# Kernel tuning notes

Measured on AMD Instinct MI355X. Metric: run time of the kernel, lower is better.

## Reference

```python
import jax, jax.numpy as jnp
import numpy as np

B, T, E, H, V = 64, 21, 512, 512, 10000


def _lstm_step(x, h, c, W_ih, W_hh, b):
    # PyTorch LSTMCell gate order: i, f, g, o
    gates = x @ W_ih.T + h @ W_hh.T + b  # [B, 4H]
    i, f, g, o = jnp.split(gates, 4, axis=-1)
    i, f, o = jax.nn.sigmoid(i), jax.nn.sigmoid(f), jax.nn.sigmoid(o)
    g = jnp.tanh(g)
    c_new = f * c + i * g
    h_new = o * jnp.tanh(c_new)
    return h_new, c_new


def setup_inputs() -> dict:
    key = jax.random.key(0)
    ks = jax.random.split(key, 8)
    s_ih = 1.0 / np.sqrt(H)
    return {
        "features": jax.random.normal(ks[0], (B, E), jnp.float32),
        "caption_embedding": jax.random.normal(ks[1], (B, T, E), jnp.float32),
        "W_ih": jax.random.uniform(ks[2], (4 * H, E), jnp.float32, -s_ih, s_ih),
        "W_hh": jax.random.uniform(ks[3], (4 * H, H), jnp.float32, -s_ih, s_ih),
        "b_ih": jax.random.uniform(ks[4], (4 * H,), jnp.float32, -s_ih, s_ih),
        "b_hh": jax.random.uniform(ks[5], (4 * H,), jnp.float32, -s_ih, s_ih),
        "W_lin": jax.random.uniform(ks[6], (V, H), jnp.float32, -s_ih, s_ih),
        "b_lin": jax.random.uniform(ks[7], (V,), jnp.float32, -s_ih, s_ih),
    }


def reference(features, caption_embedding, W_ih, W_hh, b_ih, b_hh, W_lin, b_lin):
    b = b_ih + b_hh
    batch = features.shape[0]
    hidden = W_hh.shape[1]
    h0 = jnp.zeros((batch, hidden), features.dtype)
    c0 = jnp.zeros((batch, hidden), features.dtype)
    # t = 0: consume image features, no output emitted
    h, c = _lstm_step(features, h0, c0, W_ih, W_hh, b)
    # t = 1..T-1: consume caption_embedding[:, t-1], emit linear(h)
    emb_seq = jnp.swapaxes(caption_embedding[:, :-1, :], 0, 1)  # [T-1, B, E]

    def body(carry, x_t):
        h, c = carry
        h, c = _lstm_step(x_t, h, c, W_ih, W_hh, b)
        out = h @ W_lin.T + b_lin  # [B, V]
        return (h, c), out

    _, outs = jax.lax.scan(body, (h, c), emb_seq)  # [T-1, B, V]
    return jnp.swapaxes(outs, 0, 1)  # [B, T-1, V]
```

## Files before the change

kernel.cpp:

```cpp
#include <hip/hip_runtime.h>
#include <hip/hip_bf16.h>


#define NB 64
#define NT 21
#define NE 512
#define NH 512
#define NV 10000
#define G4 2048
#define FLGD 16

typedef __attribute__((ext_vector_type(8))) short bf16x8;
typedef __attribute__((ext_vector_type(4))) float f32x4;
typedef __attribute__((ext_vector_type(4))) unsigned short u16x4;

#define OFF_WIH_HI   0UL
#define OFF_WIH_LO   2097152UL
#define OFF_WHH_HI   4194304UL
#define OFF_WHH_LO   6291456UL
#define OFF_WLIN_HI  8388608UL
#define OFF_XSEQ_HI  18743296UL
#define OFF_XSEQ_LO  20185088UL
#define OFF_BIAS     21626880UL
#define OFF_XIH      21635072UL
#define OFF_GHH      32645120UL
#define OFF_GHL      32776192UL
#define OFF_C        32907264UL
#define OFF_HBUF     33038336UL
#define OFF_FLG      34349056UL

__device__ inline unsigned short f2bf(float f) {
    unsigned int u = __float_as_uint(f);
    unsigned int r = u + 0x7FFFu + ((u >> 16) & 1u);
    return (unsigned short)(r >> 16);
}
__device__ inline float bf2f(unsigned short s) {
    return __uint_as_float(((unsigned int)s) << 16);
}

__device__ __forceinline__ void gl_lds16(const unsigned short* g, unsigned short* l) {
    auto gp = (const __attribute__((address_space(1))) unsigned int*)(unsigned long long)(const void*)g;
    auto lp = (__attribute__((address_space(3))) unsigned int*)(unsigned int)(unsigned long long)(void*)l;
    __builtin_amdgcn_global_load_lds(gp, lp, 16, 0, 0);
}

__device__ __forceinline__ void gl_lds16_sc(const unsigned short* g, unsigned short* l) {
    auto gp = (const __attribute__((address_space(1))) unsigned int*)(unsigned long long)(const void*)g;
    auto lp = (__attribute__((address_space(3))) unsigned int*)(unsigned int)(unsigned long long)(void*)l;
    __builtin_amdgcn_global_load_lds(gp, lp, 16, 0, 17);
}

__device__ __forceinline__ void st4_sc(unsigned int* p, unsigned int v) {
    asm volatile("global_store_dword %0, %1, off sc0 sc1" :: "v"(p), "v"(v) : "memory");
}

__global__ __launch_bounds__(256) void prep_kernel(
    const float* __restrict__ features, const float* __restrict__ cap,
    const float* __restrict__ W_ih, const float* __restrict__ W_hh,
    const float* __restrict__ b_ih, const float* __restrict__ b_hh,
    const float* __restrict__ W_lin, unsigned char* __restrict__ ws)
{
    const int idx = blockIdx.x * 256 + threadIdx.x;
    unsigned short* wih_hi = (unsigned short*)(ws + OFF_WIH_HI);
    unsigned short* wih_lo = (unsigned short*)(ws + OFF_WIH_LO);
    unsigned short* whh_hi = (unsigned short*)(ws + OFF_WHH_HI);
    unsigned short* whh_lo = (unsigned short*)(ws + OFF_WHH_LO);
    unsigned short* wlin_hi = (unsigned short*)(ws + OFF_WLIN_HI);
    unsigned short* xs_hi = (unsigned short*)(ws + OFF_XSEQ_HI);
    unsigned short* xs_lo = (unsigned short*)(ws + OFF_XSEQ_LO);
    float* bias = (float*)(ws + OFF_BIAS);

    if (idx < 262144) {
        const int i4 = idx * 4;
        float4 w = *(const float4*)(W_ih + i4);
        u16x4 hi, lo;
        hi.x = f2bf(w.x); lo.x = f2bf(w.x - bf2f(hi.x));
        hi.y = f2bf(w.y); lo.y = f2bf(w.y - bf2f(hi.y));
        hi.z = f2bf(w.z); lo.z = f2bf(w.z - bf2f(hi.z));
        hi.w = f2bf(w.w); lo.w = f2bf(w.w - bf2f(hi.w));
        *(u16x4*)(wih_hi + i4) = hi;
        *(u16x4*)(wih_lo + i4) = lo;
    } else if (idx < 524288) {
        const int i4 = (idx - 262144) * 4;
        float4 w = *(const float4*)(W_hh + i4);
        u16x4 hi, lo;
        hi.x = f2bf(w.x); lo.x = f2bf(w.x - bf2f(hi.x));
        hi.y = f2bf(w.y); lo.y = f2bf(w.y - bf2f(hi.y));
        hi.z = f2bf(w.z); lo.z = f2bf(w.z - bf2f(hi.z));
        hi.w = f2bf(w.w); lo.w = f2bf(w.w - bf2f(hi.w));
        *(u16x4*)(whh_hi + i4) = hi;
        *(u16x4*)(whh_lo + i4) = lo;
    } else if (idx < 1804288) {
        const int i4 = (idx - 524288) * 4;
        float4 w = *(const float4*)(W_lin + i4);
        u16x4 hi;
        hi.x = f2bf(w.x); hi.y = f2bf(w.y); hi.z = f2bf(w.z); hi.w = f2bf(w.w);
        *(u16x4*)(wlin_hi + i4) = hi;
    } else if (idx < 1976320) {
        const int i4 = (idx - 1804288) * 4;
        const int e = i4 & 511;
        const int b = (i4 >> 9) & 63;
        const int t = i4 >> 15;
        float4 x = (t == 0) ? *(const float4*)(features + b * NE + e)
                            : *(const float4*)(cap + b * (NT * NE) + (t - 1) * NE + e);
        u16x4 hi, lo;
        hi.x = f2bf(x.x); lo.x = f2bf(x.x - bf2f(hi.x));
        hi.y = f2bf(x.y); lo.y = f2bf(x.y - bf2f(hi.y));
        hi.z = f2bf(x.z); lo.z = f2bf(x.z - bf2f(hi.z));
        hi.w = f2bf(x.w); lo.w = f2bf(x.w - bf2f(hi.w));
        *(u16x4*)(xs_hi + i4) = hi;
        *(u16x4*)(xs_lo + i4) = lo;
    } else if (idx < 1976832) {
        const int j = (idx - 1976320) * 4;
        float4 a = *(const float4*)(b_ih + j);
        float4 b = *(const float4*)(b_hh + j);
        *(float4*)(bias + j) = make_float4(a.x + b.x, a.y + b.y, a.z + b.z, a.w + b.w);
    }
}

__global__ __launch_bounds__(256) void gemm_a_kernel(unsigned char* __restrict__ ws)
{
    __shared__ unsigned short Ah[2][4096], Al[2][4096], Bh[2][4096], Bl[2][4096];
    const int tid = threadIdx.x;
    const int lane = tid & 63, wv = tid >> 6;
    const int mf = lane & 15, kg = lane >> 4;
    const int mw = (wv >> 1) * 64, nw = (wv & 1) * 64;
    const int m0 = blockIdx.y * 128, n0 = blockIdx.x * 128;

    const unsigned short* __restrict__ xh = (const unsigned short*)(ws + OFF_XSEQ_HI);
    const unsigned short* __restrict__ xl = (const unsigned short*)(ws + OFF_XSEQ_LO);
    const unsigned short* __restrict__ wh = (const unsigned short*)(ws + OFF_WIH_HI);
    const unsigned short* __restrict__ wl = (const unsigned short*)(ws + OFF_WIH_LO);
    const float* __restrict__ bias = (const float*)(ws + OFF_BIAS);
    float* __restrict__ xih = (float*)(ws + OFF_XIH);

    f32x4 acc[4][4];
#pragma unroll
    for (int i = 0; i < 4; i++)
#pragma unroll
        for (int j = 0; j < 4; j++) acc[i][j] = (f32x4){0.f, 0.f, 0.f, 0.f};

    auto stage = [&](int buf, int k0) {
#pragma unroll
        for (int h = 0; h < 2; ++h) {
            int s = h * 256 + tid;
            int r = s >> 2, ks = (s & 3) * 8;
            gl_lds16(xh + (size_t)(m0 + r) * 512 + k0 + ks, &Ah[buf][s * 8]);
            gl_lds16(xl + (size_t)(m0 + r) * 512 + k0 + ks, &Al[buf][s * 8]);
            gl_lds16(wh + (size_t)(n0 + r) * 512 + k0 + ks, &Bh[buf][s * 8]);
            gl_lds16(wl + (size_t)(n0 + r) * 512 + k0 + ks, &Bl[buf][s * 8]);
        }
    };

    stage(0, 0);
    for (int kt = 0; kt < 16; ++kt) {
        __syncthreads();
        const int cur = kt & 1;
        if (kt < 15) stage(cur ^ 1, (kt + 1) * 32);
        bf16x8 ah[4], al[4], bh[4], bl[4];
#pragma unroll
        for (int i = 0; i < 4; i++) {
            ah[i] = *(const bf16x8*)&Ah[cur][(mw + i * 16 + mf) * 32 + kg * 8];
            al[i] = *(const bf16x8*)&Al[cur][(mw + i * 16 + mf) * 32 + kg * 8];
            bh[i] = *(const bf16x8*)&Bh[cur][(nw + i * 16 + mf) * 32 + kg * 8];
            bl[i] = *(const bf16x8*)&Bl[cur][(nw + i * 16 + mf) * 32 + kg * 8];
        }
#pragma unroll
        for (int i = 0; i < 4; i++)
#pragma unroll
            for (int j = 0; j < 4; j++) {
                acc[i][j] = __builtin_amdgcn_mfma_f32_16x16x32_bf16(ah[i], bh[j], acc[i][j], 0, 0, 0);
                acc[i][j] = __builtin_amdgcn_mfma_f32_16x16x32_bf16(ah[i], bl[j], acc[i][j], 0, 0, 0);
                acc[i][j] = __builtin_amdgcn_mfma_f32_16x16x32_bf16(al[i], bh[j], acc[i][j], 0, 0, 0);
            }
    }
#pragma unroll
    for (int i = 0; i < 4; i++)
#pragma unroll
        for (int j = 0; j < 4; j++) {
            const int col = n0 + nw + j * 16 + mf;
            const float bb = bias[col];
#pragma unroll
            for (int r = 0; r < 4; r++) {
                const int R = m0 + mw + i * 16 + kg * 4 + r;
                if (R < NT * NB) xih[(size_t)R * G4 + col] = acc[i][j][r] + bb;
            }
        }
}

__global__ __launch_bounds__(512, 2) void fused_persistent(
    unsigned char* __restrict__ ws, const float* __restrict__ b_lin, float* __restrict__ out)
{
    __shared__ unsigned short Hhi[64 * 512];
    __shared__ unsigned short Hlo[64 * 512];
    __shared__ float glf[4096];
    const int tid = threadIdx.x;
    const int lane = tid & 63, wv = tid >> 6;
    const int mf = lane & 15, kg = lane >> 4;

    unsigned int* __restrict__ flg = (unsigned int*)(ws + OFF_C);
    unsigned short* __restrict__ hbuf = (unsigned short*)(ws + OFF_HBUF);
    const unsigned short* __restrict__ wlin = (const unsigned short*)(ws + OFF_WLIN_HI);

    if (blockIdx.x < 32) {
        const int bc = blockIdx.x;
        const int q = wv & 3;
        const int mh = wv >> 2;

        unsigned short* __restrict__ ghh = (unsigned short*)(ws + OFF_GHH);
        unsigned short* __restrict__ ghl = (unsigned short*)(ws + OFF_GHL);
        const unsigned short* __restrict__ whh_hi = (const unsigned short*)(ws + OFF_WHH_HI);
        const unsigned short* __restrict__ whh_lo = (const unsigned short*)(ws + OFF_WHH_LO);
        const float* __restrict__ xih_base = (const float*)(ws + OFF_XIH);

        bf16x8 bh[16], blo[16];
#pragma unroll
        for (int j = 0; j < 16; ++j) {
            const size_t off = (size_t)(q * 512 + bc * 16 + mf) * 512 + j * 32 + kg * 8;
            bh[j] = *(const bf16x8*)(whh_hi + off);
            blo[j] = *(const bf16x8*)(whh_lo + off);
        }

        const int crow = tid >> 3;
        const int cp = tid & 7;
        const int c0 = bc * 16 + cp * 2;
        const int jc0 = c0 >> 3;
        float creg0 = 0.f, creg1 = 0.f;

        float2 xp[4];
        auto load_xp = [&](int tt) {
            const float* __restrict__ xq = xih_base + (size_t)tt * NB * G4;
#pragma unroll
            for (int g2 = 0; g2 < 4; ++g2)
                xp[g2] = *(const float2*)&xq[crow * G4 + g2 * 512 + c0];
        };
        load_xp(0);

        for (int t = 0; t < NT; ++t) {
            f32x4 acc[2];
            acc[0] = (f32x4){0.f, 0.f, 0.f, 0.f};
            acc[1] = (f32x4){0.f, 0.f, 0.f, 0.f};

            if (t > 0) {
                const int rd = (t + 1) & 1;
                const unsigned short* __restrict__ ghh_r = ghh + rd * (NB * NH);
                const unsigned short* __restrict__ ghl_r = ghl + rd * (NB * NH);
#pragma unroll
                for (int i = 0; i < 8; ++i) {
                    const int s = i * 512 + tid;
                    gl_lds16_sc(ghh_r + s * 8, &Hhi[s * 8]);
                }
#pragma unroll
                for (int i = 0; i < 8; ++i) {
                    const int s = i * 512 + tid;
                    gl_lds16_sc(ghl_r + s * 8, &Hlo[s * 8]);
                }
                asm volatile("s_waitcnt vmcnt(8)" ::: "memory");
                __builtin_amdgcn_s_barrier();
#pragma unroll
                for (int kt = 0; kt < 16; ++kt) {
                    const int j = kt * 4 + kg;
#pragma unroll
                    for (int m = 0; m < 2; ++m) {
                        const int row = mh * 32 + m * 16 + mf;
                        bf16x8 a_hi = *(const bf16x8*)&Hhi[(row * 64 + (j ^ (row & 7))) * 8];
                        acc[m] = __builtin_amdgcn_mfma_f32_16x16x32_bf16(a_hi, bh[kt], acc[m], 0, 0, 0);
                        acc[m] = __builtin_amdgcn_mfma_f32_16x16x32_bf16(a_hi, blo[kt], acc[m], 0, 0, 0);
                    }
                }
                asm volatile("s_waitcnt vmcnt(0)" ::: "memory");
                __builtin_amdgcn_s_barrier();
#pragma unroll
                for (int kt = 0; kt < 16; ++kt) {
                    const int j = kt * 4 + kg;
#pragma unroll
                    for (int m = 0; m < 2; ++m) {
                        const int row = mh * 32 + m * 16 + mf;
                        bf16x8 a_lo = *(const bf16x8*)&Hlo[(row * 64 + (j ^ (row & 7))) * 8];
                        acc[m] = __builtin_amdgcn_mfma_f32_16x16x32_bf16(a_lo, bh[kt], acc[m], 0, 0, 0);
                    }
                }
            }

#pragma unroll
            for (int m = 0; m < 2; ++m) {
                const int row = mh * 32 + m * 16 + kg * 4;
#pragma unroll
                for (int r = 0; r < 4; ++r)
                    glf[(q * 64 + row + r) * 16 + mf] = acc[m][r];
            }
            __syncthreads();

            {
                unsigned short* __restrict__ ghh_w = ghh + (t & 1) * (NB * NH);
                unsigned short* __restrict__ ghl_w = ghl + (t & 1) * (NB * NH);
                const float2 g0 = *(const float2*)&glf[(0 * 64 + crow) * 16 + cp * 2];
                const float2 g1 = *(const float2*)&glf[(1 * 64 + crow) * 16 + cp * 2];
                const float2 g2 = *(const float2*)&glf[(2 * 64 + crow) * 16 + cp * 2];
                const float2 g3 = *(const float2*)&glf[(3 * 64 + crow) * 16 + cp * 2];
                const float gi0 = g0.x + xp[0].x, gi1 = g0.y + xp[0].y;
                const float gf0 = g1.x + xp[1].x, gf1 = g1.y + xp[1].y;
                const float gg0 = g2.x + xp[2].x, gg1 = g2.y + xp[2].y;
                const float go0 = g3.x + xp[3].x, go1 = g3.y + xp[3].y;
                const float i0 = 1.f / (1.f + __expf(-gi0)), i1 = 1.f / (1.f + __expf(-gi1));
                const float f0 = 1.f / (1.f + __expf(-gf0)), f1 = 1.f / (1.f + __expf(-gf1));
                const float ga0 = tanhf(gg0),                ga1 = tanhf(gg1);
                const float o0 = 1.f / (1.f + __expf(-go0)), o1 = 1.f / (1.f + __expf(-go1));
                const float cn0 = f0 * creg0 + i0 * ga0;
                const float cn1 = f1 * creg1 + i1 * ga1;
                creg0 = cn0; creg1 = cn1;
                const float h0 = o0 * tanhf(cn0);
                const float h1 = o1 * tanhf(cn1);
                const unsigned short hi0 = f2bf(h0), hi1 = f2bf(h1);
                const unsigned short lo0 = f2bf(h0 - bf2f(hi0)), lo1 = f2bf(h1 - bf2f(hi1));
                const unsigned int hpack = (unsigned int)hi0 | ((unsigned int)hi1 << 16);
                const unsigned int lpack = (unsigned int)lo0 | ((unsigned int)lo1 << 16);
                const int sw = crow * 512 + ((jc0 ^ (crow & 7)) << 3) + (cp & 3) * 2;
                st4_sc((unsigned int*)&ghh_w[sw], hpack);
                st4_sc((unsigned int*)&ghl_w[sw], lpack);
                if (t >= 1)
                    st4_sc((unsigned int*)&hbuf[(size_t)(t - 1) * (NB * NH) + crow * NH + c0], hpack);
            }

            asm volatile("s_waitcnt vmcnt(0)" ::: "memory");
            __syncthreads();
            if (tid == 0) {
                unsigned int one = 1u;
                unsigned int* fp = flg + ((size_t)t * 32 + bc) * FLGD;
                asm volatile("global_store_dword %0, %1, off sc0 sc1" :: "v"(fp), "v"(one) : "memory");
            }
            if (t < NT - 1) {
                load_xp(t + 1);
                if (wv == 0) {
                    const unsigned int* fp = flg + ((size_t)t * 32 + (lane & 31)) * FLGD;
                    while (__hip_atomic_load(fp, __ATOMIC_RELAXED, __HIP_MEMORY_SCOPE_AGENT) == 0u)
                        __builtin_amdgcn_s_sleep(1);
                }
                __syncthreads();
            }
        }
        asm volatile("s_waitcnt vmcnt(0)" ::: "memory");
        return;
    }

    const int g = blockIdx.x - 32;
    const int jt = g % 79;
    const int rshare = g / 79;
    const int nshare = (jt < 66) ? 3 : 2;
    const int n0g = jt * 128;
    const int mw2 = (wv >> 2) * 32, nw2 = (wv & 3) * 32;

    unsigned short* __restrict__ AsB = Hhi;
    unsigned short* __restrict__ BsB = Hhi + 4096;

    for (int tt = rshare; tt < NT - 1; tt += nshare) {
        if (wv == 0) {
            const unsigned int* fp = flg + ((size_t)(tt + 1) * 32 + (lane & 31)) * FLGD;
            while (__hip_atomic_load(fp, __ATOMIC_RELAXED, __HIP_MEMORY_SCOPE_AGENT) == 0u)
                __builtin_amdgcn_s_sleep(2);
        }
        __syncthreads();

        const unsigned short* __restrict__ hbA = hbuf + (size_t)tt * (NB * NH);
        auto stageC = [&](int buf, int k0) {
            if (tid < 256) {
                const int s = tid;
                const int r = s >> 2, kcol = (s & 3) * 8;
                gl_lds16_sc(hbA + (size_t)r * 512 + k0 + kcol, &AsB[buf * 2048 + s * 8]);
            } else {
#pragma unroll
                for (int h2 = 0; h2 < 2; ++h2) {
                    const int s = h2 * 256 + (tid - 256);
                    const int r = s >> 2, kcol = (s & 3) * 8;
                    gl_lds16(wlin + (size_t)(n0g + r) * 512 + k0 + kcol, &BsB[buf * 4096 + s * 8]);
                }
            }
        };

        f32x4 acc2[2][2];
#pragma unroll
        for (int i = 0; i < 2; i++)
#pragma unroll
            for (int j = 0; j < 2; j++) acc2[i][j] = (f32x4){0.f, 0.f, 0.f, 0.f};

        stageC(0, 0);
        for (int kt = 0; kt < 16; ++kt) {
            __syncthreads();
            const int cur = kt & 1;
            if (kt < 15) stageC(cur ^ 1, (kt + 1) * 32);
            bf16x8 af[2], bfv[2];
#pragma unroll
            for (int i = 0; i < 2; i++) {
                af[i]  = *(const bf16x8*)&AsB[cur * 2048 + (mw2 + i * 16 + mf) * 32 + kg * 8];
                bfv[i] = *(const bf16x8*)&BsB[cur * 4096 + (nw2 + i * 16 + mf) * 32 + kg * 8];
            }
#pragma unroll
            for (int i = 0; i < 2; i++)
#pragma unroll
                for (int j = 0; j < 2; j++)
                    acc2[i][j] = __builtin_amdgcn_mfma_f32_16x16x32_bf16(af[i], bfv[j], acc2[i][j], 0, 0, 0);
        }
#pragma unroll
        for (int i = 0; i < 2; i++)
#pragma unroll
            for (int j = 0; j < 2; j++) {
                const int col = n0g + nw2 + j * 16 + mf;
                if (col < NV) {
                    const float bl = b_lin[col];
#pragma unroll
                    for (int r = 0; r < 4; r++) {
                        const int b_ = mw2 + i * 16 + kg * 4 + r;
                        out[(size_t)b_ * ((NT - 1) * NV) + (size_t)tt * NV + col] = acc2[i][j][r] + bl;
                    }
                }
            }
        __syncthreads();
    }
}

extern "C" void kernel_launch(void* const* d_in, const int* in_sizes, int n_in,
                              void* d_out, int out_size, void* d_ws, size_t ws_size,
                              hipStream_t stream)
{
    const float* features = (const float*)d_in[0];
    const float* cap      = (const float*)d_in[1];
    const float* W_ih     = (const float*)d_in[2];
    const float* W_hh     = (const float*)d_in[3];
    const float* b_ih     = (const float*)d_in[4];
    const float* b_hh     = (const float*)d_in[5];
    const float* W_lin    = (const float*)d_in[6];
    const float* b_lin    = (const float*)d_in[7];
    float* out = (float*)d_out;
    unsigned char* ws = (unsigned char*)d_ws;

    hipMemsetAsync(ws + OFF_C, 0, (size_t)NT * 32 * FLGD * sizeof(unsigned int), stream);

    hipLaunchKernelGGL(prep_kernel, dim3(7722), dim3(256), 0, stream,
                       features, cap, W_ih, W_hh, b_ih, b_hh, W_lin, ws);
    hipLaunchKernelGGL(gemm_a_kernel, dim3(16, 11), dim3(256), 0, stream, ws);
    hipLaunchKernelGGL(fused_persistent, dim3(256), dim3(512), 0, stream, ws, b_lin, out);
}
```

Baseline: 257.8 us.

## Fuse input-projection GEMM into persistent kernel with per-slab readiness counters

Removes the separate gemm_a kernel launch: the 224 output-GEMM blocks of the persistent kernel first compute the x@W_ih projection per 64-row timestep slab and bump a per-slab counter, which the recurrent blocks wait on before loading each step's projection. W_hh split into bf16 hi/lo is moved out of the prep kernel and done in registers inside the recurrent blocks. This saves a kernel launch and lets the projection overlap with the recurrence. In exchange it adds spin-wait dependencies, and the recurrent blocks may stall early if slab 0 is not ready. The launch-bounds occupancy hint of 2 blocks is also dropped.

```diff
diff --git a/kernel.cpp b/kernel.cpp
--- a/kernel.cpp
+++ b/kernel.cpp
@@ -56,15 +56,13 @@
 
 __global__ __launch_bounds__(256) void prep_kernel(
     const float* __restrict__ features, const float* __restrict__ cap,
-    const float* __restrict__ W_ih, const float* __restrict__ W_hh,
-    const float* __restrict__ b_ih, const float* __restrict__ b_hh,
-    const float* __restrict__ W_lin, unsigned char* __restrict__ ws)
+    const float* __restrict__ W_ih, const float* __restrict__ b_ih,
+    const float* __restrict__ b_hh, const float* __restrict__ W_lin,
+    unsigned char* __restrict__ ws)
 {
     const int idx = blockIdx.x * 256 + threadIdx.x;
     unsigned short* wih_hi = (unsigned short*)(ws + OFF_WIH_HI);
     unsigned short* wih_lo = (unsigned short*)(ws + OFF_WIH_LO);
-    unsigned short* whh_hi = (unsigned short*)(ws + OFF_WHH_HI);
-    unsigned short* whh_lo = (unsigned short*)(ws + OFF_WHH_LO);
     unsigned short* wlin_hi = (unsigned short*)(ws + OFF_WLIN_HI);
     unsigned short* xs_hi = (unsigned short*)(ws + OFF_XSEQ_HI);
     unsigned short* xs_lo = (unsigned short*)(ws + OFF_XSEQ_LO);
@@ -80,24 +78,14 @@
         hi.w = f2bf(w.w); lo.w = f2bf(w.w - bf2f(hi.w));
         *(u16x4*)(wih_hi + i4) = hi;
         *(u16x4*)(wih_lo + i4) = lo;
-    } else if (idx < 524288) {
+    } else if (idx < 1542144) {
         const int i4 = (idx - 262144) * 4;
-        float4 w = *(const float4*)(W_hh + i4);
-        u16x4 hi, lo;
-        hi.x = f2bf(w.x); lo.x = f2bf(w.x - bf2f(hi.x));
-        hi.y = f2bf(w.y); lo.y = f2bf(w.y - bf2f(hi.y));
-        hi.z = f2bf(w.z); lo.z = f2bf(w.z - bf2f(hi.z));
-        hi.w = f2bf(w.w); lo.w = f2bf(w.w - bf2f(hi.w));
-        *(u16x4*)(whh_hi + i4) = hi;
-        *(u16x4*)(whh_lo + i4) = lo;
-    } else if (idx < 1804288) {
-        const int i4 = (idx - 524288) * 4;
         float4 w = *(const float4*)(W_lin + i4);
         u16x4 hi;
         hi.x = f2bf(w.x); hi.y = f2bf(w.y); hi.z = f2bf(w.z); hi.w = f2bf(w.w);
         *(u16x4*)(wlin_hi + i4) = hi;
-    } else if (idx < 1976320) {
-        const int i4 = (idx - 1804288) * 4;
+    } else if (idx < 1714176) {
+        const int i4 = (idx - 1542144) * 4;
         const int e = i4 & 511;
         const int b = (i4 >> 9) & 63;
         const int t = i4 >> 15;
@@ -110,86 +98,17 @@
         hi.w = f2bf(x.w); lo.w = f2bf(x.w - bf2f(hi.w));
         *(u16x4*)(xs_hi + i4) = hi;
         *(u16x4*)(xs_lo + i4) = lo;
-    } else if (idx < 1976832) {
-        const int j = (idx - 1976320) * 4;
+    } else if (idx < 1714688) {
+        const int j = (idx - 1714176) * 4;
         float4 a = *(const float4*)(b_ih + j);
         float4 b = *(const float4*)(b_hh + j);
         *(float4*)(bias + j) = make_float4(a.x + b.x, a.y + b.y, a.z + b.z, a.w + b.w);
     }
 }
 
-__global__ __launch_bounds__(256) void gemm_a_kernel(unsigned char* __restrict__ ws)
-{
-    __shared__ unsigned short Ah[2][4096], Al[2][4096], Bh[2][4096], Bl[2][4096];
-    const int tid = threadIdx.x;
-    const int lane = tid & 63, wv = tid >> 6;
-    const int mf = lane & 15, kg = lane >> 4;
-    const int mw = (wv >> 1) * 64, nw = (wv & 1) * 64;
-    const int m0 = blockIdx.y * 128, n0 = blockIdx.x * 128;
-
-    const unsigned short* __restrict__ xh = (const unsigned short*)(ws + OFF_XSEQ_HI);
-    const unsigned short* __restrict__ xl = (const unsigned short*)(ws + OFF_XSEQ_LO);
-    const unsigned short* __restrict__ wh = (const unsigned short*)(ws + OFF_WIH_HI);
-    const unsigned short* __restrict__ wl = (const unsigned short*)(ws + OFF_WIH_LO);
-    const float* __restrict__ bias = (const float*)(ws + OFF_BIAS);
-    float* __restrict__ xih = (float*)(ws + OFF_XIH);
-
-    f32x4 acc[4][4];
-#pragma unroll
-    for (int i = 0; i < 4; i++)
-#pragma unroll
-        for (int j = 0; j < 4; j++) acc[i][j] = (f32x4){0.f, 0.f, 0.f, 0.f};
-
-    auto stage = [&](int buf, int k0) {
-#pragma unroll
-        for (int h = 0; h < 2; ++h) {
-            int s = h * 256 + tid;
-            int r = s >> 2, ks = (s & 3) * 8;
-            gl_lds16(xh + (size_t)(m0 + r) * 512 + k0 + ks, &Ah[buf][s * 8]);
-            gl_lds16(xl + (size_t)(m0 + r) * 512 + k0 + ks, &Al[buf][s * 8]);
-            gl_lds16(wh + (size_t)(n0 + r) * 512 + k0 + ks, &Bh[buf][s * 8]);
-            gl_lds16(wl + (size_t)(n0 + r) * 512 + k0 + ks, &Bl[buf][s * 8]);
-        }
-    };
-
-    stage(0, 0);
-    for (int kt = 0; kt < 16; ++kt) {
-        __syncthreads();
-        const int cur = kt & 1;
-        if (kt < 15) stage(cur ^ 1, (kt + 1) * 32);
-        bf16x8 ah[4], al[4], bh[4], bl[4];
-#pragma unroll
-        for (int i = 0; i < 4; i++) {
-            ah[i] = *(const bf16x8*)&Ah[cur][(mw + i * 16 + mf) * 32 + kg * 8];
-            al[i] = *(const bf16x8*)&Al[cur][(mw + i * 16 + mf) * 32 + kg * 8];
-            bh[i] = *(const bf16x8*)&Bh[cur][(nw + i * 16 + mf) * 32 + kg * 8];
-            bl[i] = *(const bf16x8*)&Bl[cur][(nw + i * 16 + mf) * 32 + kg * 8];
-        }
-#pragma unroll
-        for (int i = 0; i < 4; i++)
-#pragma unroll
-            for (int j = 0; j < 4; j++) {
-                acc[i][j] = __builtin_amdgcn_mfma_f32_16x16x32_bf16(ah[i], bh[j], acc[i][j], 0, 0, 0);
-                acc[i][j] = __builtin_amdgcn_mfma_f32_16x16x32_bf16(ah[i], bl[j], acc[i][j], 0, 0, 0);
-                acc[i][j] = __builtin_amdgcn_mfma_f32_16x16x32_bf16(al[i], bh[j], acc[i][j], 0, 0, 0);
-            }
-    }
-#pragma unroll
-    for (int i = 0; i < 4; i++)
-#pragma unroll
-        for (int j = 0; j < 4; j++) {
-            const int col = n0 + nw + j * 16 + mf;
-            const float bb = bias[col];
-#pragma unroll
-            for (int r = 0; r < 4; r++) {
-                const int R = m0 + mw + i * 16 + kg * 4 + r;
-                if (R < NT * NB) xih[(size_t)R * G4 + col] = acc[i][j][r] + bb;
-            }
-        }
-}
-
-__global__ __launch_bounds__(512, 2) void fused_persistent(
-    unsigned char* __restrict__ ws, const float* __restrict__ b_lin, float* __restrict__ out)
+__global__ __launch_bounds__(512) void fused_persistent(
+    unsigned char* __restrict__ ws, const float* __restrict__ W_hh_f,
+    const float* __restrict__ b_lin, float* __restrict__ out)
 {
     __shared__ unsigned short Hhi[64 * 512];
     __shared__ unsigned short Hlo[64 * 512];
@@ -199,8 +118,11 @@
     const int mf = lane & 15, kg = lane >> 4;
 
     unsigned int* __restrict__ flg = (unsigned int*)(ws + OFF_C);
+    unsigned int* __restrict__ slabctr = (unsigned int*)(ws + OFF_FLG);
     unsigned short* __restrict__ hbuf = (unsigned short*)(ws + OFF_HBUF);
     const unsigned short* __restrict__ wlin = (const unsigned short*)(ws + OFF_WLIN_HI);
+    const float* __restrict__ bias = (const float*)(ws + OFF_BIAS);
+    float* __restrict__ xih_base = (float*)(ws + OFF_XIH);
 
     if (blockIdx.x < 32) {
         const int bc = blockIdx.x;
@@ -209,16 +131,20 @@
 
         unsigned short* __restrict__ ghh = (unsigned short*)(ws + OFF_GHH);
         unsigned short* __restrict__ ghl = (unsigned short*)(ws + OFF_GHL);
-        const unsigned short* __restrict__ whh_hi = (const unsigned short*)(ws + OFF_WHH_HI);
-        const unsigned short* __restrict__ whh_lo = (const unsigned short*)(ws + OFF_WHH_LO);
-        const float* __restrict__ xih_base = (const float*)(ws + OFF_XIH);
 
         bf16x8 bh[16], blo[16];
 #pragma unroll
         for (int j = 0; j < 16; ++j) {
-            const size_t off = (size_t)(q * 512 + bc * 16 + mf) * 512 + j * 32 + kg * 8;
-            bh[j] = *(const bf16x8*)(whh_hi + off);
-            blo[j] = *(const bf16x8*)(whh_lo + off);
+            const float* src = W_hh_f + (size_t)(q * 512 + bc * 16 + mf) * 512 + j * 32 + kg * 8;
+            float4 w0 = *(const float4*)src;
+            float4 w1 = *(const float4*)(src + 4);
+            float ff[8] = {w0.x, w0.y, w0.z, w0.w, w1.x, w1.y, w1.z, w1.w};
+#pragma unroll
+            for (int e = 0; e < 8; ++e) {
+                const unsigned short h = f2bf(ff[e]);
+                bh[j][e] = (short)h;
+                blo[j][e] = (short)f2bf(ff[e] - bf2f(h));
+            }
         }
 
         const int crow = tid >> 3;
@@ -234,6 +160,12 @@
             for (int g2 = 0; g2 < 4; ++g2)
                 xp[g2] = *(const float2*)&xq[crow * G4 + g2 * 512 + c0];
         };
+
+        if (tid == 0) {
+            while (__hip_atomic_load(&slabctr[0], __ATOMIC_RELAXED, __HIP_MEMORY_SCOPE_AGENT) < 16u)
+                __builtin_amdgcn_s_sleep(1);
+        }
+        __syncthreads();
         load_xp(0);
 
         for (int t = 0; t < NT; ++t) {
@@ -330,6 +262,11 @@
                 asm volatile("global_store_dword %0, %1, off sc0 sc1" :: "v"(fp), "v"(one) : "memory");
             }
             if (t < NT - 1) {
+                if (tid == 0) {
+                    while (__hip_atomic_load(&slabctr[(t + 1) * FLGD], __ATOMIC_RELAXED, __HIP_MEMORY_SCOPE_AGENT) < 16u)
+                        __builtin_amdgcn_s_sleep(1);
+                }
+                __syncthreads();
                 load_xp(t + 1);
                 if (wv == 0) {
                     const unsigned int* fp = flg + ((size_t)t * 32 + (lane & 31)) * FLGD;
@@ -344,11 +281,94 @@
     }
 
     const int g = blockIdx.x - 32;
+    const int mw2 = (wv >> 2) * 32, nw2 = (wv & 3) * 32;
+
+    {
+        const unsigned short* __restrict__ xh = (const unsigned short*)(ws + OFF_XSEQ_HI);
+        const unsigned short* __restrict__ xl = (const unsigned short*)(ws + OFF_XSEQ_LO);
+        const unsigned short* __restrict__ wih_h = (const unsigned short*)(ws + OFF_WIH_HI);
+        const unsigned short* __restrict__ wih_l = (const unsigned short*)(ws + OFF_WIH_LO);
+
+        unsigned short* Ah2 = Hhi;
+        unsigned short* Al2 = Hhi + 4096;
+        unsigned short* Bh2 = Hhi + 8192;
+        unsigned short* Bl2 = Hhi + 16384;
+
+        const int ntile = (g < 112) ? 2 : 1;
+        for (int p = 0; p < ntile; ++p) {
+            const int T = (p == 0) ? g : 224 + g;
+            const int slab = T >> 4, ct = T & 15;
+            const unsigned short* __restrict__ xhA = xh + (size_t)slab * 64 * 512;
+            const unsigned short* __restrict__ xlA = xl + (size_t)slab * 64 * 512;
+
+            auto stageA = [&](int buf, int k0) {
+                if (tid < 256) {
+                    const int s = tid, r = s >> 2, kc = (s & 3) * 8;
+                    gl_lds16(xhA + (size_t)r * 512 + k0 + kc, &Ah2[buf * 2048 + s * 8]);
+                    gl_lds16(xlA + (size_t)r * 512 + k0 + kc, &Al2[buf * 2048 + s * 8]);
+                } else {
+#pragma unroll
+                    for (int h2 = 0; h2 < 2; ++h2) {
+                        const int s = h2 * 256 + (tid - 256), r = s >> 2, kc = (s & 3) * 8;
+                        gl_lds16(wih_h + (size_t)(ct * 128 + r) * 512 + k0 + kc, &Bh2[buf * 4096 + s * 8]);
+                        gl_lds16(wih_l + (size_t)(ct * 128 + r) * 512 + k0 + kc, &Bl2[buf * 4096 + s * 8]);
+                    }
+                }
+            };
+
+            f32x4 acc2[2][2];
+#pragma unroll
+            for (int i = 0; i < 2; i++)
+#pragma unroll
+                for (int j = 0; j < 2; j++) acc2[i][j] = (f32x4){0.f, 0.f, 0.f, 0.f};
+
+            stageA(0, 0);
+            for (int kt = 0; kt < 16; ++kt) {
+                __syncthreads();
+                const int cur = kt & 1;
+                if (kt < 15) stageA(cur ^ 1, (kt + 1) * 32);
+                bf16x8 ah_[2], al_[2], bh_[2], bl_[2];
+#pragma unroll
+                for (int i = 0; i < 2; i++) {
+                    ah_[i] = *(const bf16x8*)&Ah2[cur * 2048 + (mw2 + i * 16 + mf) * 32 + kg * 8];
+                    al_[i] = *(const bf16x8*)&Al2[cur * 2048 + (mw2 + i * 16 + mf) * 32 + kg * 8];
+                    bh_[i] = *(const bf16x8*)&Bh2[cur * 4096 + (nw2 + i * 16 + mf) * 32 + kg * 8];
+                    bl_[i] = *(const bf16x8*)&Bl2[cur * 4096 + (nw2 + i * 16 + mf) * 32 + kg * 8];
+                }
+#pragma unroll
+                for (int i = 0; i < 2; i++)
+#pragma unroll
+                    for (int j = 0; j < 2; j++) {
+                        acc2[i][j] = __builtin_amdgcn_mfma_f32_16x16x32_bf16(ah_[i], bh_[j], acc2[i][j], 0, 0, 0);
+                        acc2[i][j] = __builtin_amdgcn_mfma_f32_16x16x32_bf16(ah_[i], bl_[j], acc2[i][j], 0, 0, 0);
+                        acc2[i][j] = __builtin_amdgcn_mfma_f32_16x16x32_bf16(al_[i], bh_[j], acc2[i][j], 0, 0, 0);
+                    }
+            }
+#pragma unroll
+            for (int i = 0; i < 2; i++)
+#pragma unroll
+                for (int j = 0; j < 2; j++) {
+                    const int col = ct * 128 + nw2 + j * 16 + mf;
+                    const float bb = bias[col];
+#pragma unroll
+                    for (int r = 0; r < 4; r++) {
+                        const int row = slab * 64 + mw2 + i * 16 + kg * 4 + r;
+                        st4_sc((unsigned int*)&xih_base[(size_t)row * G4 + col],
+                               __float_as_uint(acc2[i][j][r] + bb));
+                    }
+                }
+            asm volatile("s_waitcnt vmcnt(0)" ::: "memory");
+            __syncthreads();
+            if (tid == 0)
+                __hip_atomic_fetch_add(&slabctr[slab * FLGD], 1u, __ATOMIC_RELAXED, __HIP_MEMORY_SCOPE_AGENT);
+            __syncthreads();
+        }
+    }
+
     const int jt = g % 79;
     const int rshare = g / 79;
     const int nshare = (jt < 66) ? 3 : 2;
     const int n0g = jt * 128;
-    const int mw2 = (wv >> 2) * 32, nw2 = (wv & 3) * 32;
 
     unsigned short* __restrict__ AsB = Hhi;
     unsigned short* __restrict__ BsB = Hhi + 4096;
@@ -434,9 +454,9 @@
     unsigned char* ws = (unsigned char*)d_ws;
 
     hipMemsetAsync(ws + OFF_C, 0, (size_t)NT * 32 * FLGD * sizeof(unsigned int), stream);
-
-    hipLaunchKernelGGL(prep_kernel, dim3(7722), dim3(256), 0, stream,
-                       features, cap, W_ih, W_hh, b_ih, b_hh, W_lin, ws);
-    hipLaunchKernelGGL(gemm_a_kernel, dim3(16, 11), dim3(256), 0, stream, ws);
-    hipLaunchKernelGGL(fused_persistent, dim3(256), dim3(512), 0, stream, ws, b_lin, out);
-}
+    hipMemsetAsync(ws + OFF_FLG, 0, (size_t)NT * FLGD * sizeof(unsigned int), stream);
+
+    hipLaunchKernelGGL(prep_kernel, dim3(6698), dim3(256), 0, stream,
+                       features, cap, W_ih, b_ih, b_hh, W_lin, ws);
+    hipLaunchKernelGGL(fused_persistent, dim3(256), dim3(512), 0, stream, ws, W_hh, b_lin, out);
+}
```

New measurement: 251.0 us. -2.6%, faster.
